# Kernel optimization log

Measured on AMD Instinct MI355X. Metric: run time of the kernel, lower is better.

The kernel has to match this reference:

```python
import jax, jax.numpy as jnp
import numpy as np

MOMENTUM = 0.9
EPS_MASK = 1e-6   # torch clamp(min=1e-6) on mask sum
EPS_NORM = 1e-12  # torch F.normalize eps

def _l2norm(x):
    n = jnp.linalg.norm(x, axis=-1, keepdims=True)
    return x / jnp.maximum(n, EPS_NORM)

def setup_inputs() -> dict:
    key = jax.random.key(0)
    k1, k2, k3, k4, k5 = jax.random.split(key, 5)
    num_users, num_proto, embd_dim = 50000, 16, 128
    B, S = 8192, 50
    return {
        "user_prototypes": jax.random.normal(k1, (num_users, num_proto, embd_dim), jnp.float32),
        "shared_prototypes": jax.random.normal(k2, (1, num_proto, embd_dim), jnp.float32),
        "interaction_count": jax.random.uniform(k3, (num_users,), jnp.float32),
        "features": jax.random.normal(k4, (B, S, embd_dim), jnp.float32),
        "success_mask": jax.random.uniform(k5, (B, S), jnp.float32),
        "user_idx": jnp.arange(B, dtype=jnp.int64) if jax.config.jax_enable_x64 else jnp.arange(B, dtype=jnp.int32),
    }

def reference(user_prototypes, shared_prototypes, interaction_count, features, success_mask, user_idx):
    # --- gather ---
    current = user_prototypes[user_idx]                    # [B, P, D]
    ic = interaction_count[user_idx]                       # [B]
    m = jnp.clip(MOMENTUM + ic / 1000.0, MOMENTUM, 0.99)[:, None, None]
    # --- masked reduction over history (features dim==3 branch, mask dim==2) ---
    mask = success_mask[..., None]                         # [B, S, 1]
    upd = (features * mask).sum(axis=1) / jnp.maximum(mask.sum(axis=1), EPS_MASK)  # [B, D]
    upd = _l2norm(upd)                                     # F.normalize(dim=-1)
    upd = jnp.broadcast_to(upd[:, None, :], current.shape) # expand to [B, P, D]
    # --- momentum blend + scatter write ---
    new_batch = m * current + (1.0 - m) * upd
    new_user_prototypes = user_prototypes.at[user_idx].set(new_batch)
    # --- shared prototype update ---
    shared_upd = _l2norm(upd.mean(axis=0))                 # [P, D]
    new_shared = MOMENTUM * shared_prototypes + (1.0 - MOMENTUM) * shared_upd[None]
    # --- interaction count increment ---
    new_ic = interaction_count.at[user_idx].add(1.0)
    return new_user_prototypes, new_shared, new_ic
```

## Files before the change

kernel.cpp:

```cpp
#include <hip/hip_runtime.h>

#define NB 8192
#define NS 50
#define ND 128
#define NP 16
#define NU 50000
#define NRED 64

__global__ void k_init_map(int* __restrict__ map) {
    int i = blockIdx.x * blockDim.x + threadIdx.x;
    if (i < NU) map[i] = -1;
}

__global__ void k_scatter_map(const int* __restrict__ user_idx, int* __restrict__ map) {
    int b = blockIdx.x * blockDim.x + threadIdx.x;
    if (b < NB) map[user_idx[b]] = b;
}

__global__ __launch_bounds__(256) void k_big(
    const float* __restrict__ proto,
    const float* __restrict__ ic,
    const float* __restrict__ features,
    const float* __restrict__ mask,
    const int* __restrict__ map,
    float* __restrict__ out_proto,
    float* __restrict__ out_ic,
    float* __restrict__ upd)
{
    int u = blockIdx.x;
    int t = threadIdx.x;
    int b = map[u];

    const float4* proto4 = (const float4*)proto;
    float4* out4 = (float4*)out_proto;
    size_t base = (size_t)u * (NP * ND / 4);

    if (b < 0) {
        out4[base + t]       = proto4[base + t];
        out4[base + t + 256] = proto4[base + t + 256];
        if (t == 0) out_ic[u] = ic[u];
        return;
    }

    __shared__ float  smask[NS];
    __shared__ float4 part[8][32];
    __shared__ float4 updv[32];

    if (t < NS) smask[t] = mask[(size_t)b * NS + t];
    __syncthreads();

    int q = t & 31;
    int g = t >> 5;
    const float4* f4 = (const float4*)features + (size_t)b * (NS * ND / 4);
    float4 acc = {0.f, 0.f, 0.f, 0.f};
    for (int s = g; s < NS; s += 8) {
        float w = smask[s];
        float4 v = f4[s * 32 + q];
        acc.x += v.x * w; acc.y += v.y * w; acc.z += v.z * w; acc.w += v.w * w;
    }
    part[g][q] = acc;
    __syncthreads();

    if (t < 32) {
        float msum = 0.f;
#pragma unroll
        for (int s = 0; s < NS; ++s) msum += smask[s];

        float4 a = part[0][t];
#pragma unroll
        for (int g2 = 1; g2 < 8; ++g2) {
            float4 p = part[g2][t];
            a.x += p.x; a.y += p.y; a.z += p.z; a.w += p.w;
        }
        float invm = 1.0f / fmaxf(msum, 1e-6f);
        a.x *= invm; a.y *= invm; a.z *= invm; a.w *= invm;

        float d2 = a.x * a.x + a.y * a.y + a.z * a.z + a.w * a.w;
#pragma unroll
        for (int mm = 16; mm >= 1; mm >>= 1) d2 += __shfl_xor(d2, mm, 64);
        float inv = 1.0f / fmaxf(sqrtf(d2), 1e-12f);
        a.x *= inv; a.y *= inv; a.z *= inv; a.w *= inv;

        updv[t] = a;
        ((float4*)upd)[(size_t)b * 32 + t] = a;
    }
    __syncthreads();

    float icv = ic[u];
    float m = fminf(fmaxf(0.9f + icv * 0.001f, 0.9f), 0.99f);
    float om = 1.0f - m;
    if (t == 0) out_ic[u] = icv + 1.0f;

#pragma unroll
    for (int rep = 0; rep < 2; ++rep) {
        int idx = t + rep * 256;
        float4 v = proto4[base + idx];
        float4 uu = updv[idx & 31];
        v.x = m * v.x + om * uu.x;
        v.y = m * v.y + om * uu.y;
        v.z = m * v.z + om * uu.z;
        v.w = m * v.w + om * uu.w;
        out4[base + idx] = v;
    }
}

__global__ void k_colsum(const float* __restrict__ upd, float* __restrict__ part) {
    int blk = blockIdx.x;
    int t = threadIdx.x;
    int d = t & 127;
    int h = t >> 7;

    const int rows = NB / NRED;
    int r0 = blk * rows;

    float s = 0.f;
    for (int r = r0 + h; r < r0 + rows; r += 2)
        s += upd[(size_t)r * ND + d];

    __shared__ float red[2][ND];
    red[h][d] = s;
    __syncthreads();
    if (h == 0)
        part[(size_t)blk * ND + d] = red[0][d] + red[1][d];
}

__global__ void k_shared_final(const float* __restrict__ part,
                               const float* __restrict__ shared_in,
                               float* __restrict__ shared_out) {
    int d = threadIdx.x;

    float tot = 0.f;
#pragma unroll
    for (int j = 0; j < NRED; ++j) tot += part[(size_t)j * ND + d];
    float mean = tot / (float)NB;

    __shared__ float red[ND];
    red[d] = mean * mean;
    __syncthreads();
    for (int off = 64; off > 0; off >>= 1) {
        if (d < off) red[d] += red[d + off];
        __syncthreads();
    }
    float inv = 1.0f / fmaxf(sqrtf(red[0]), 1e-12f);
    float su = mean * inv;

#pragma unroll
    for (int p = 0; p < NP; ++p)
        shared_out[p * ND + d] = 0.9f * shared_in[p * ND + d] + 0.1f * su;
}

extern "C" void kernel_launch(void* const* d_in, const int* in_sizes, int n_in,
                              void* d_out, int out_size, void* d_ws, size_t ws_size,
                              hipStream_t stream) {
    const float* user_prototypes   = (const float*)d_in[0];
    const float* shared_prototypes = (const float*)d_in[1];
    const float* interaction_count = (const float*)d_in[2];
    const float* features          = (const float*)d_in[3];
    const float* success_mask      = (const float*)d_in[4];
    const int*   user_idx          = (const int*)d_in[5];

    float* out_proto  = (float*)d_out;
    float* out_shared = out_proto + (size_t)NU * NP * ND;
    float* out_ic     = out_shared + NP * ND;

    int*   map  = (int*)d_ws;
    float* upd  = (float*)((char*)d_ws + 200704);
    float* part = upd + (size_t)NB * ND;

    k_init_map<<<(NU + 255) / 256, 256, 0, stream>>>(map);
    k_scatter_map<<<(NB + 255) / 256, 256, 0, stream>>>(user_idx, map);

    k_big<<<NU, 256, 0, stream>>>(user_prototypes, interaction_count,
                                  features, success_mask, map,
                                  out_proto, out_ic, upd);

    k_colsum<<<NRED, 256, 0, stream>>>(upd, part);
    k_shared_final<<<1, ND, 0, stream>>>(part, shared_prototypes, out_shared);
}
```

Baseline: 224.1 us.

## Drop map init kernel via validated map lookup; use nontemporal loads/stores

Removes the kernel that filled the user→batch map with -1. The main kernel now checks each map entry it reads for range and confirms user_idx[b]==u, so uninitialized workspace is safe to read. All streaming prototype and feature accesses now use nontemporal load/store builtins on native vector types, to reduce cache pollution. NRED is doubled for the column-sum stage. This costs one extra dependent global read per mapped block and depends on the validation handling stale workspace contents correctly.

```diff
diff --git a/kernel.cpp b/kernel.cpp
--- a/kernel.cpp
+++ b/kernel.cpp
@@ -5,12 +5,9 @@
 #define ND 128
 #define NP 16
 #define NU 50000
-#define NRED 64
+#define NRED 128
 
-__global__ void k_init_map(int* __restrict__ map) {
-    int i = blockIdx.x * blockDim.x + threadIdx.x;
-    if (i < NU) map[i] = -1;
-}
+typedef float f4v __attribute__((ext_vector_type(4)));
 
 __global__ void k_scatter_map(const int* __restrict__ user_idx, int* __restrict__ map) {
     int b = blockIdx.x * blockDim.x + threadIdx.x;
@@ -23,40 +20,46 @@
     const float* __restrict__ features,
     const float* __restrict__ mask,
     const int* __restrict__ map,
+    const int* __restrict__ user_idx,
     float* __restrict__ out_proto,
     float* __restrict__ out_ic,
     float* __restrict__ upd)
 {
     int u = blockIdx.x;
     int t = threadIdx.x;
+
     int b = map[u];
+    bool mapped = (b >= 0) && (b < NB);
+    if (mapped) mapped = (user_idx[b] == u);
 
-    const float4* proto4 = (const float4*)proto;
-    float4* out4 = (float4*)out_proto;
+    const f4v* proto4 = (const f4v*)proto;
+    f4v* out4 = (f4v*)out_proto;
     size_t base = (size_t)u * (NP * ND / 4);
 
-    if (b < 0) {
-        out4[base + t]       = proto4[base + t];
-        out4[base + t + 256] = proto4[base + t + 256];
+    if (!mapped) {
+        f4v v0 = __builtin_nontemporal_load(&proto4[base + t]);
+        f4v v1 = __builtin_nontemporal_load(&proto4[base + t + 256]);
+        __builtin_nontemporal_store(v0, &out4[base + t]);
+        __builtin_nontemporal_store(v1, &out4[base + t + 256]);
         if (t == 0) out_ic[u] = ic[u];
         return;
     }
 
-    __shared__ float  smask[NS];
-    __shared__ float4 part[8][32];
-    __shared__ float4 updv[32];
+    __shared__ float smask[NS];
+    __shared__ f4v   part[8][32];
+    __shared__ f4v   updv[32];
 
     if (t < NS) smask[t] = mask[(size_t)b * NS + t];
     __syncthreads();
 
     int q = t & 31;
     int g = t >> 5;
-    const float4* f4 = (const float4*)features + (size_t)b * (NS * ND / 4);
-    float4 acc = {0.f, 0.f, 0.f, 0.f};
+    const f4v* f4 = (const f4v*)features + (size_t)b * (NS * ND / 4);
+    f4v acc = {0.f, 0.f, 0.f, 0.f};
     for (int s = g; s < NS; s += 8) {
         float w = smask[s];
-        float4 v = f4[s * 32 + q];
-        acc.x += v.x * w; acc.y += v.y * w; acc.z += v.z * w; acc.w += v.w * w;
+        f4v v = __builtin_nontemporal_load(&f4[s * 32 + q]);
+        acc += v * w;
     }
     part[g][q] = acc;
     __syncthreads();
@@ -66,23 +69,19 @@
 #pragma unroll
         for (int s = 0; s < NS; ++s) msum += smask[s];
 
-        float4 a = part[0][t];
+        f4v a = part[0][t];
 #pragma unroll
-        for (int g2 = 1; g2 < 8; ++g2) {
-            float4 p = part[g2][t];
-            a.x += p.x; a.y += p.y; a.z += p.z; a.w += p.w;
-        }
-        float invm = 1.0f / fmaxf(msum, 1e-6f);
-        a.x *= invm; a.y *= invm; a.z *= invm; a.w *= invm;
+        for (int g2 = 1; g2 < 8; ++g2) a += part[g2][t];
+
+        a *= (1.0f / fmaxf(msum, 1e-6f));
 
         float d2 = a.x * a.x + a.y * a.y + a.z * a.z + a.w * a.w;
 #pragma unroll
         for (int mm = 16; mm >= 1; mm >>= 1) d2 += __shfl_xor(d2, mm, 64);
-        float inv = 1.0f / fmaxf(sqrtf(d2), 1e-12f);
-        a.x *= inv; a.y *= inv; a.z *= inv; a.w *= inv;
+        a *= (1.0f / fmaxf(sqrtf(d2), 1e-12f));
 
         updv[t] = a;
-        ((float4*)upd)[(size_t)b * 32 + t] = a;
+        ((f4v*)upd)[(size_t)b * 32 + t] = a;
     }
     __syncthreads();
 
@@ -94,13 +93,10 @@
 #pragma unroll
     for (int rep = 0; rep < 2; ++rep) {
         int idx = t + rep * 256;
-        float4 v = proto4[base + idx];
-        float4 uu = updv[idx & 31];
-        v.x = m * v.x + om * uu.x;
-        v.y = m * v.y + om * uu.y;
-        v.z = m * v.z + om * uu.z;
-        v.w = m * v.w + om * uu.w;
-        out4[base + idx] = v;
+        f4v v = __builtin_nontemporal_load(&proto4[base + idx]);
+        f4v uu = updv[idx & 31];
+        v = m * v + om * uu;
+        __builtin_nontemporal_store(v, &out4[base + idx]);
     }
 }
 
@@ -167,11 +163,10 @@
     float* upd  = (float*)((char*)d_ws + 200704);
     float* part = upd + (size_t)NB * ND;
 
-    k_init_map<<<(NU + 255) / 256, 256, 0, stream>>>(map);
     k_scatter_map<<<(NB + 255) / 256, 256, 0, stream>>>(user_idx, map);
 
     k_big<<<NU, 256, 0, stream>>>(user_prototypes, interaction_count,
-                                  features, success_mask, map,
+                                  features, success_mask, map, user_idx,
                                   out_proto, out_ic, upd);
 
     k_colsum<<<NRED, 256, 0, stream>>>(upd, part);
```

Result: faster. 189.8 us (-15.3%).
